# Optimization experiments

Measured on AMD Instinct MI355X. Metric: run time of the kernel, lower is better.

The kernel has to match this reference:

```python
import jax, jax.numpy as jnp
import numpy as np

B, S, P, E, H, NCTX = 4, 1024, 1024, 1024, 16, 2048
D = E // H


def setup_inputs() -> dict:
    key = jax.random.key(0)
    k0, k1, k2, k3 = jax.random.split(key, 4)
    x = jax.random.normal(k0, (B, S, E), jnp.float32)
    layer_past = jax.random.normal(k1, (2, B, H, P, D), jnp.float32)
    w_attn = jax.random.normal(k2, (E, 3 * E), jnp.float32) * 0.02
    b_attn = jnp.zeros((3 * E,), jnp.float32)
    w_proj = jax.random.normal(k3, (E, E), jnp.float32) * 0.02
    b_proj = jnp.zeros((E,), jnp.float32)
    return {"x": x, "layer_past": layer_past, "w_attn": w_attn,
            "b_attn": b_attn, "w_proj": w_proj, "b_proj": b_proj}


def reference(x, layer_past, w_attn, b_attn, w_proj, b_proj):
    # c_attn: Conv1D == linear with weight [nx, nf]
    qkv = x @ w_attn + b_attn                       # [B,S,3E]
    q, k, v = jnp.split(qkv, 3, axis=-1)

    def heads(t):                                   # [B,S,E] -> [B,H,S,D]
        return t.reshape(B, -1, H, D).transpose(0, 2, 1, 3)

    q, k, v = heads(q), heads(k), heads(v)
    # KV-cache concat: layer_past[0] is [B,H,P,D] (module transposes to
    # [B,H,D,P] then concats on last dim; equivalent to concat on seq dim).
    k = jnp.concatenate([layer_past[0], k], axis=2)  # [B,H,ns,D]
    v = jnp.concatenate([layer_past[1], v], axis=2)  # [B,H,ns,D]
    present = jnp.stack([k, v])                      # [2,B,H,ns,D]

    nd, ns = q.shape[2], k.shape[2]
    w = jnp.einsum('bhqd,bhkd->bhqk', q, k) / jnp.sqrt(jnp.float32(D))
    mask = jnp.tril(jnp.ones((NCTX, NCTX), jnp.float32))[ns - nd:ns, :ns]
    w = w * mask - 10000.0 * (1.0 - mask)
    a = jnp.einsum('bhqk,bhkd->bhqd', jax.nn.softmax(w, axis=-1), v)
    a = a.transpose(0, 2, 1, 3).reshape(B, -1, E)    # merge heads
    out = a @ w_proj + b_proj
    return out, present
```

## Files before the change

kernel.cpp:

```cpp
#include <hip/hip_runtime.h>
#include <hip/hip_bf16.h>

#define BB 4
#define SS 1024
#define PP 1024
#define EE 1024
#define HH 16
#define DD 64
#define NS 2048
#define E3 3072
#define VOFF 8388608
#define VPAST 4194304

typedef __attribute__((ext_vector_type(8))) short short8;
typedef __attribute__((ext_vector_type(4))) float floatx4;
typedef __attribute__((ext_vector_type(16))) float floatx16;
typedef __attribute__((ext_vector_type(4))) unsigned uintx4;

__device__ __forceinline__ short f2bf(float f) {
    return (short)(__bfloat16_as_ushort(__float2bfloat16(f)));
}

__device__ __forceinline__ unsigned cvtpk(float lo, float hi) {
    unsigned r;
    asm("v_cvt_pk_bf16_f32 %0, %1, %2" : "=v"(r) : "v"(lo), "v"(hi));
    return r;
}

__device__ __forceinline__ void plswap(unsigned &a, unsigned &b) {
    asm("v_permlane32_swap_b32 %0, %1" : "+v"(a), "+v"(b));
}

__device__ __forceinline__ void gload16(const void* g, void* l) {
    __builtin_amdgcn_global_load_lds(
        (const __attribute__((address_space(1))) void*)g,
        (__attribute__((address_space(3))) void*)l, 16, 0, 0);
}

__global__ __launch_bounds__(256) void cvt_copy_k(
    const float* __restrict__ x, const float* __restrict__ past,
    short* __restrict__ xb, short* __restrict__ kbp, short* __restrict__ vbp,
    float* __restrict__ present)
{
    size_t e0 = ((size_t)blockIdx.x * 256 + threadIdx.x) * 8;
    if (e0 < 4194304) {
        float4 a0 = *(const float4*)(x + e0);
        float4 a1 = *(const float4*)(x + e0 + 4);
        short8 s;
        s[0] = f2bf(a0.x); s[1] = f2bf(a0.y); s[2] = f2bf(a0.z); s[3] = f2bf(a0.w);
        s[4] = f2bf(a1.x); s[5] = f2bf(a1.y); s[6] = f2bf(a1.z); s[7] = f2bf(a1.w);
        *(short8*)(xb + e0) = s;
    } else {
        size_t r = e0 - 4194304;
        int sec = (r >= 4194304);
        if (sec) r -= 4194304;
        const float* src = past + (sec ? VPAST : 0) + r;
        int row = (int)(r >> 6);
        int bh = row >> 10, t = row & 1023, d = (int)(r & 63);
        size_t off = ((size_t)bh * NS + t) * DD + d;
        float4 a0 = *(const float4*)src;
        float4 a1 = *(const float4*)(src + 4);
        short8 s;
        s[0] = f2bf(a0.x); s[1] = f2bf(a0.y); s[2] = f2bf(a0.z); s[3] = f2bf(a0.w);
        s[4] = f2bf(a1.x); s[5] = f2bf(a1.y); s[6] = f2bf(a1.z); s[7] = f2bf(a1.w);
        *(short8*)((sec ? vbp : kbp) + off) = s;
        float* pd = present + (sec ? VOFF : 0) + off;
        *(float4*)(pd)     = a0;
        *(float4*)(pd + 4) = a1;
    }
}

__global__ __launch_bounds__(256) void wtrans_k(
    const float* __restrict__ wa, const float* __restrict__ wp,
    short* __restrict__ wab, short* __restrict__ wpb)
{
    __shared__ short Ts[64][72];
    int bid = blockIdx.x;
    const float* src; short* dst; int n0, k0, Nsrc;
    if (bid < 768) { k0 = (bid & 15) * 64; n0 = (bid >> 4) * 64; src = wa; dst = wab; Nsrc = E3; }
    else { bid -= 768; k0 = (bid & 15) * 64; n0 = (bid >> 4) * 64; src = wp; dst = wpb; Nsrc = EE; }
    int tid = threadIdx.x;
    int r = tid >> 2, c = (tid & 3) * 16;
    const float* s = src + (size_t)(k0 + r) * Nsrc + n0 + c;
    float4 a0 = *(const float4*)(s);
    float4 a1 = *(const float4*)(s + 4);
    float4 a2 = *(const float4*)(s + 8);
    float4 a3 = *(const float4*)(s + 12);
    Ts[c +  0][r] = f2bf(a0.x); Ts[c +  1][r] = f2bf(a0.y);
    Ts[c +  2][r] = f2bf(a0.z); Ts[c +  3][r] = f2bf(a0.w);
    Ts[c +  4][r] = f2bf(a1.x); Ts[c +  5][r] = f2bf(a1.y);
    Ts[c +  6][r] = f2bf(a1.z); Ts[c +  7][r] = f2bf(a1.w);
    Ts[c +  8][r] = f2bf(a2.x); Ts[c +  9][r] = f2bf(a2.y);
    Ts[c + 10][r] = f2bf(a2.z); Ts[c + 11][r] = f2bf(a2.w);
    Ts[c + 12][r] = f2bf(a3.x); Ts[c + 13][r] = f2bf(a3.y);
    Ts[c + 14][r] = f2bf(a3.z); Ts[c + 15][r] = f2bf(a3.w);
    __syncthreads();
    int n = tid >> 2, kc = (tid & 3) * 16;
    short8 v0 = *(const short8*)&Ts[n][kc];
    short8 v1 = *(const short8*)&Ts[n][kc + 8];
    short* d = dst + (size_t)(n0 + n) * EE + k0 + kc;
    *(short8*)d = v0;
    *(short8*)(d + 8) = v1;
}

template<int MODE, int NT>
__global__ __launch_bounds__(256) void gemm_bt_k(
    const short* __restrict__ A,
    const short* __restrict__ Bt,
    const float* __restrict__ bias,
    float* __restrict__ outf,
    short* __restrict__ qb, short* __restrict__ kbp, short* __restrict__ vbp,
    float* __restrict__ present,
    int N)
{
    constexpr int MR = (NT == 128) ? 4 : 2;
    __shared__ __align__(16) short As[128 * 32];
    __shared__ __align__(16) short Bs[NT * 32];
    int tid = threadIdx.x;
    int wave = tid >> 6, lane = tid & 63;
    int fr = lane & 15, quad = lane >> 4;
    int wm = (NT == 128) ? (wave >> 1) : wave;
    int wn = (NT == 128) ? (wave & 1) : 0;
    int hw = blockIdx.y * gridDim.x + blockIdx.x;
    int nwg = gridDim.x * gridDim.y;
    int work = (hw & 7) * (nwg >> 3) + (hw >> 3);
    int bx = work / gridDim.y, by = work - bx * gridDim.y;
    int m0 = bx * 128, n0 = by * NT;

    floatx4 acc[MR][4];
#pragma unroll
    for (int m = 0; m < MR; ++m)
#pragma unroll
        for (int n = 0; n < 4; ++n) acc[m][n] = (floatx4){0.f, 0.f, 0.f, 0.f};

    for (int k0 = 0; k0 < 1024; k0 += 32) {
        __syncthreads();
#pragma unroll
        for (int p = 0; p < 2; ++p) {
            int idx = p * 256 + tid;
            int row = idx >> 2, ch = idx & 3;
            gload16(A + (size_t)(m0 + row) * 1024 + k0 + ch * 8,
                    As + (p * 256 + wave * 64) * 8);
        }
#pragma unroll
        for (int p = 0; p < NT / 64; ++p) {
            int idx = p * 256 + tid;
            int row = idx >> 2, ch = idx & 3;
            gload16(Bt + (size_t)(n0 + row) * 1024 + k0 + ch * 8,
                    Bs + (p * 256 + wave * 64) * 8);
        }
        __syncthreads();
        short8 af[MR], bf[4];
#pragma unroll
        for (int m = 0; m < MR; ++m)
            af[m] = *(const short8*)(As + (wm * (MR * 16) + m * 16 + fr) * 32 + quad * 8);
#pragma unroll
        for (int n = 0; n < 4; ++n)
            bf[n] = *(const short8*)(Bs + (wn * 64 + n * 16 + fr) * 32 + quad * 8);
#pragma unroll
        for (int m = 0; m < MR; ++m)
#pragma unroll
            for (int n = 0; n < 4; ++n)
                acc[m][n] = __builtin_amdgcn_mfma_f32_16x16x32_bf16(af[m], bf[n], acc[m][n], 0, 0, 0);
    }
#pragma unroll
    for (int n = 0; n < 4; ++n) {
        int gc = n0 + wn * 64 + n * 16 + fr;
        float bv = bias[gc];
#pragma unroll
        for (int m = 0; m < MR; ++m) {
#pragma unroll
            for (int r = 0; r < 4; ++r) {
                int gr = m0 + wm * (MR * 16) + m * 16 + quad * 4 + r;
                float val = acc[m][n][r] + bv;
                if (MODE == 1) {
                    outf[(size_t)gr * N + gc] = val;
                } else {
                    int sec = gc >> 10, h = (gc >> 6) & 15, d = gc & 63;
                    int b = gr >> 10, sq = gr & 1023;
                    size_t bh = (size_t)(b * HH + h);
                    if (sec == 0) {
                        qb[(bh * SS + sq) * DD + d] = f2bf(val * 0.18033688f);
                    } else {
                        size_t off = (bh * NS + PP + sq) * DD + d;
                        if (sec == 1) { present[off] = val;        kbp[off] = f2bf(val); }
                        else          { present[VOFF + off] = val; vbp[off] = f2bf(val); }
                    }
                }
            }
        }
    }
}

__global__ __launch_bounds__(256) void flash_attn_k(
    const short* __restrict__ qb, const short* __restrict__ kbp,
    const short* __restrict__ vbp, short* __restrict__ ab)
{
    __shared__ __align__(16) short smem[16384];
    short* Ks = smem;
    short* Vs = smem + 8192;

    int tid = threadIdx.x;
    int wave = tid >> 6, lane = tid & 63;
    int qcol = lane & 31, hi = lane >> 5;

    int bid = blockIdx.x;
    int work = (bid & 7) * 64 + (bid >> 3);
    int bh = work >> 3;
    int q0 = (work & 7) * 128;

    const short* qrow = qb + ((size_t)bh * SS + q0 + wave * 32 + qcol) * DD + hi * 8;
    short8 qf[4];
#pragma unroll
    for (int i = 0; i < 4; ++i) qf[i] = *(const short8*)(qrow + i * 16);

    const short* kbase = kbp + (size_t)bh * NS * DD;
    const short* vbase = vbp + (size_t)bh * NS * DD;

    float m_r = -1e30f, l_r = 0.f;
    floatx16 Oa[2];
#pragma unroll
    for (int dt = 0; dt < 2; ++dt)
#pragma unroll
        for (int r = 0; r < 16; ++r) Oa[dt][r] = 0.f;

    int vkey = lane, vd0 = (tid >> 6) * 16;
    int qminw = PP + q0 + wave * 32;
    int qmaxw = qminw + 31;

    int nchunks = 18 + (q0 >> 6);
    short8 vs0, vs1;

    auto KISSUE = [&](int cc, int bufi) {
        const short* kc = kbase + (size_t)cc * 64 * DD;
        short* Kd = Ks + bufi * 4096;
#pragma unroll
        for (int p = 0; p < 2; ++p) {
            int idx = p * 256 + tid;
            int row = idx >> 3, ch = idx & 7;
            gload16(kc + row * 64 + ((ch ^ (row & 7)) * 8), Kd + (p * 256 + wave * 64) * 8);
        }
    };
    auto VLOAD = [&](int cc) {
        const short* src = vbase + ((size_t)cc * 64 + vkey) * DD + vd0;
        vs0 = *(const short8*)src;
        vs1 = *(const short8*)(src + 8);
    };
    auto VWRITE = [&](int bufi) {
        short* Vd = Vs + bufi * 4096;
#pragma unroll
        for (int i = 0; i < 8; ++i) {
            int d0i = vd0 + i, d1i = vd0 + 8 + i;
            Vd[d0i * 64 + (((vkey >> 3) ^ (d0i & 7)) << 3) + (vkey & 7)] = vs0[i];
            Vd[d1i * 64 + (((vkey >> 3) ^ (d1i & 7)) << 3) + (vkey & 7)] = vs1[i];
        }
    };

    KISSUE(0, 0); VLOAD(0); VWRITE(0);
    __syncthreads();

    for (int c = 0; c < nchunks; ++c) {
        int t0 = c * 64;
        int cur = c & 1;
        KISSUE(c + 1, cur ^ 1);
        VLOAD(c + 1);
        if (t0 <= qmaxw) {
            const short* Kc = Ks + cur * 4096;
            const short* Vc = Vs + cur * 4096;
            floatx16 Sa[2];
#pragma unroll
            for (int ct = 0; ct < 2; ++ct)
#pragma unroll
                for (int r = 0; r < 16; ++r) Sa[ct][r] = 0.f;
#pragma unroll
            for (int ct = 0; ct < 2; ++ct) {
                int key = ct * 32 + qcol;
                int rbase = key * 64, rx = key & 7;
#pragma unroll
                for (int d0 = 0; d0 < 4; ++d0) {
                    short8 kf = *(const short8*)(Kc + rbase + (((d0 * 2 + hi) ^ rx) * 8));
                    Sa[ct] = __builtin_amdgcn_mfma_f32_32x32x16_bf16(kf, qf[d0], Sa[ct], 0, 0, 0);
                }
            }
            if (t0 + 63 > qminw) {
                int qa = qminw + qcol;
#pragma unroll
                for (int ct = 0; ct < 2; ++ct)
#pragma unroll
                    for (int r = 0; r < 16; ++r) {
                        int ka = t0 + ct * 32 + (r & 3) + 8 * (r >> 2) + 4 * hi;
                        if (ka > qa) Sa[ct][r] = -1e30f;
                    }
            }
            float mx0 = Sa[0][0], mx1 = Sa[0][1], mx2 = Sa[0][2], mx3 = Sa[0][3];
#pragma unroll
            for (int ct = 0; ct < 2; ++ct)
#pragma unroll
                for (int r = (ct ? 0 : 4); r < 16; r += 4) {
                    mx0 = fmaxf(mx0, Sa[ct][r]);
                    mx1 = fmaxf(mx1, Sa[ct][r + 1]);
                    mx2 = fmaxf(mx2, Sa[ct][r + 2]);
                    mx3 = fmaxf(mx3, Sa[ct][r + 3]);
                }
            float mx = fmaxf(fmaxf(mx0, mx1), fmaxf(mx2, mx3));
            mx = fmaxf(mx, __shfl_xor(mx, 32, 64));
            if (!__all(mx <= m_r + 11.5416f)) {
                float mnew = fmaxf(m_r, mx);
                float al = exp2f(m_r - mnew);
                l_r *= al;
#pragma unroll
                for (int dt = 0; dt < 2; ++dt)
#pragma unroll
                    for (int r = 0; r < 16; ++r) Oa[dt][r] *= al;
                m_r = mnew;
            }
            float s0 = 0.f, s1 = 0.f, s2 = 0.f, s3 = 0.f;
#pragma unroll
            for (int ct = 0; ct < 2; ++ct)
#pragma unroll
                for (int r = 0; r < 16; r += 4) {
                    float p0 = exp2f(Sa[ct][r]     - m_r);
                    float p1 = exp2f(Sa[ct][r + 1] - m_r);
                    float p2 = exp2f(Sa[ct][r + 2] - m_r);
                    float p3 = exp2f(Sa[ct][r + 3] - m_r);
                    Sa[ct][r] = p0; Sa[ct][r + 1] = p1; Sa[ct][r + 2] = p2; Sa[ct][r + 3] = p3;
                    s0 += p0; s1 += p1; s2 += p2; s3 += p3;
                }
            float sum = (s0 + s1) + (s2 + s3);
            sum += __shfl_xor(sum, 32, 64);
            l_r += sum;
            short8 pfr[2][2];
#pragma unroll
            for (int ct = 0; ct < 2; ++ct) {
                unsigned w0 = cvtpk(Sa[ct][0],  Sa[ct][1]);
                unsigned w2 = cvtpk(Sa[ct][4],  Sa[ct][5]);
                unsigned w1 = cvtpk(Sa[ct][2],  Sa[ct][3]);
                unsigned w3 = cvtpk(Sa[ct][6],  Sa[ct][7]);
                plswap(w0, w2);
                plswap(w1, w3);
                union { uintx4 u; short8 s; } cv0;
                cv0.u = (uintx4){w0, w1, w2, w3};
                pfr[ct][0] = cv0.s;
                unsigned x0 = cvtpk(Sa[ct][8],  Sa[ct][9]);
                unsigned x2 = cvtpk(Sa[ct][12], Sa[ct][13]);
                unsigned x1 = cvtpk(Sa[ct][10], Sa[ct][11]);
                unsigned x3 = cvtpk(Sa[ct][14], Sa[ct][15]);
                plswap(x0, x2);
                plswap(x1, x3);
                union { uintx4 u; short8 s; } cv1;
                cv1.u = (uintx4){x0, x1, x2, x3};
                pfr[ct][1] = cv1.s;
            }
#pragma unroll
            for (int ct = 0; ct < 2; ++ct)
#pragma unroll
                for (int ks = 0; ks < 2; ++ks) {
                    int chunkb = ct * 4 + ks * 2 + hi;
#pragma unroll
                    for (int dt = 0; dt < 2; ++dt) {
                        int row = dt * 32 + qcol;
                        short8 vf = *(const short8*)(Vc + row * 64 + ((chunkb ^ (row & 7)) << 3));
                        Oa[dt] = __builtin_amdgcn_mfma_f32_32x32x16_bf16(vf, pfr[ct][ks], Oa[dt], 0, 0, 0);
                    }
                }
        }
        VWRITE(cur ^ 1);
        __syncthreads();
    }
    short* Ow = smem + wave * 2304;
    float inv = 1.f / l_r;
#pragma unroll
    for (int dt = 0; dt < 2; ++dt)
#pragma unroll
        for (int r = 0; r < 16; ++r) {
            int d = dt * 32 + (r & 3) + 8 * (r >> 2) + 4 * hi;
            Ow[qcol * 72 + d] = f2bf(Oa[dt][r] * inv);
        }
    int b = bh >> 4, h = bh & 15;
    int row = lane >> 1, doff = (lane & 1) * 32;
    int qa = q0 + wave * 32 + row;
    short* dst = ab + ((size_t)(b * SS + qa)) * EE + h * DD + doff;
    const short* srcr = Ow + row * 72 + doff;
    *(short8*)(dst)      = *(const short8*)(srcr);
    *(short8*)(dst + 8)  = *(const short8*)(srcr + 8);
    *(short8*)(dst + 16) = *(const short8*)(srcr + 16);
    *(short8*)(dst + 24) = *(const short8*)(srcr + 24);
}

extern "C" void kernel_launch(void* const* d_in, const int* in_sizes, int n_in,
                              void* d_out, int out_size, void* d_ws, size_t ws_size,
                              hipStream_t stream) {
    const float* x      = (const float*)d_in[0];
    const float* past   = (const float*)d_in[1];
    const float* w_attn = (const float*)d_in[2];
    const float* b_attn = (const float*)d_in[3];
    const float* w_proj = (const float*)d_in[4];
    const float* b_proj = (const float*)d_in[5];
    float* out = (float*)d_out;
    float* present = out + (size_t)BB * SS * EE;

    short* ws  = (short*)d_ws;
    short* xb  = ws;
    short* wab = xb  + 4194304;
    short* wpb = wab + 3145728;
    short* qb  = wpb + 1048576;
    short* kbp = qb  + 4194304;
    short* vbp = kbp + 8388608;
    short* ab  = vbp + 8388608;

    cvt_copy_k<<<6144, 256, 0, stream>>>(x, past, xb, kbp, vbp, present);
    wtrans_k<<<1024, 256, 0, stream>>>(w_attn, w_proj, wab, wpb);
    gemm_bt_k<0, 128><<<dim3(32, 24), 256, 0, stream>>>(xb, wab, b_attn, nullptr,
                                                        qb, kbp, vbp, present, E3);
    flash_attn_k<<<512, 256, 0, stream>>>(qb, kbp, vbp, ab);
    gemm_bt_k<1, 64><<<dim3(32, 16), 256, 0, stream>>>(ab, wpb, b_proj, out,
                                                       nullptr, nullptr, nullptr, nullptr, EE);
}
```

Baseline: 302.4 us.

## Split attention keys across wave pairs and double-buffer GEMM LDS tiles

The flash attention block grows to 512 threads. Each pair of waves shares one 32-query group and splits every 64-key chunk into two 32-key halves. Afterward the two partial softmax states (max, sum, output) are merged through shared memory. This doubles the waves per block to raise occupancy and latency hiding, at the cost of an extra reduction epilogue with several barriers. The GEMM kernels now double-buffer their A/B LDS tiles, loading the next k-slice while computing the current one and using one barrier per iteration instead of two, which doubles LDS use.

Result: no change. 297.5 us (-1.6%).

```diff
diff --git a/kernel.cpp b/kernel.cpp
--- a/kernel.cpp
+++ b/kernel.cpp
@@ -114,8 +114,8 @@
     int N)
 {
     constexpr int MR = (NT == 128) ? 4 : 2;
-    __shared__ __align__(16) short As[128 * 32];
-    __shared__ __align__(16) short Bs[NT * 32];
+    __shared__ __align__(16) short As[2][128 * 32];
+    __shared__ __align__(16) short Bs[2][NT * 32];
     int tid = threadIdx.x;
     int wave = tid >> 6, lane = tid & 63;
     int fr = lane & 15, quad = lane >> 4;
@@ -133,35 +133,41 @@
 #pragma unroll
         for (int n = 0; n < 4; ++n) acc[m][n] = (floatx4){0.f, 0.f, 0.f, 0.f};
 
-    for (int k0 = 0; k0 < 1024; k0 += 32) {
-        __syncthreads();
+    auto STAGE = [&](int k0, int buf) {
 #pragma unroll
         for (int p = 0; p < 2; ++p) {
             int idx = p * 256 + tid;
             int row = idx >> 2, ch = idx & 3;
             gload16(A + (size_t)(m0 + row) * 1024 + k0 + ch * 8,
-                    As + (p * 256 + wave * 64) * 8);
+                    &As[buf][(p * 256 + wave * 64) * 8]);
         }
 #pragma unroll
         for (int p = 0; p < NT / 64; ++p) {
             int idx = p * 256 + tid;
             int row = idx >> 2, ch = idx & 3;
             gload16(Bt + (size_t)(n0 + row) * 1024 + k0 + ch * 8,
-                    Bs + (p * 256 + wave * 64) * 8);
+                    &Bs[buf][(p * 256 + wave * 64) * 8]);
         }
-        __syncthreads();
+    };
+
+    STAGE(0, 0);
+    __syncthreads();
+    for (int k0 = 0; k0 < 1024; k0 += 32) {
+        int cur = (k0 >> 5) & 1;
+        if (k0 + 32 < 1024) STAGE(k0 + 32, cur ^ 1);
         short8 af[MR], bf[4];
 #pragma unroll
         for (int m = 0; m < MR; ++m)
-            af[m] = *(const short8*)(As + (wm * (MR * 16) + m * 16 + fr) * 32 + quad * 8);
+            af[m] = *(const short8*)(&As[cur][(wm * (MR * 16) + m * 16 + fr) * 32 + quad * 8]);
 #pragma unroll
         for (int n = 0; n < 4; ++n)
-            bf[n] = *(const short8*)(Bs + (wn * 64 + n * 16 + fr) * 32 + quad * 8);
+            bf[n] = *(const short8*)(&Bs[cur][(wn * 64 + n * 16 + fr) * 32 + quad * 8]);
 #pragma unroll
         for (int m = 0; m < MR; ++m)
 #pragma unroll
             for (int n = 0; n < 4; ++n)
                 acc[m][n] = __builtin_amdgcn_mfma_f32_16x16x32_bf16(af[m], bf[n], acc[m][n], 0, 0, 0);
+        __syncthreads();
     }
 #pragma unroll
     for (int n = 0; n < 4; ++n) {
@@ -192,7 +198,7 @@
     }
 }
 
-__global__ __launch_bounds__(256) void flash_attn_k(
+__global__ __launch_bounds__(512) void flash_attn_k(
     const short* __restrict__ qb, const short* __restrict__ kbp,
     const short* __restrict__ vbp, short* __restrict__ ab)
 {
@@ -203,13 +209,14 @@
     int tid = threadIdx.x;
     int wave = tid >> 6, lane = tid & 63;
     int qcol = lane & 31, hi = lane >> 5;
+    int qg = wave >> 1, kh = wave & 1;
 
     int bid = blockIdx.x;
     int work = (bid & 7) * 64 + (bid >> 3);
     int bh = work >> 3;
     int q0 = (work & 7) * 128;
 
-    const short* qrow = qb + ((size_t)bh * SS + q0 + wave * 32 + qcol) * DD + hi * 8;
+    const short* qrow = qb + ((size_t)bh * SS + q0 + qg * 32 + qcol) * DD + hi * 8;
     short8 qf[4];
 #pragma unroll
     for (int i = 0; i < 4; ++i) qf[i] = *(const short8*)(qrow + i * 16);
@@ -224,84 +231,64 @@
 #pragma unroll
         for (int r = 0; r < 16; ++r) Oa[dt][r] = 0.f;
 
-    int vkey = lane, vd0 = (tid >> 6) * 16;
-    int qminw = PP + q0 + wave * 32;
+    int vkey = tid & 63, vd0 = (tid >> 6) * 8;
+    int qminw = PP + q0 + qg * 32;
     int qmaxw = qminw + 31;
 
-    int nchunks = 18 + (q0 >> 6);
-    short8 vs0, vs1;
-
+    short8 vs0;
     auto KISSUE = [&](int cc, int bufi) {
         const short* kc = kbase + (size_t)cc * 64 * DD;
-        short* Kd = Ks + bufi * 4096;
-#pragma unroll
-        for (int p = 0; p < 2; ++p) {
-            int idx = p * 256 + tid;
-            int row = idx >> 3, ch = idx & 7;
-            gload16(kc + row * 64 + ((ch ^ (row & 7)) * 8), Kd + (p * 256 + wave * 64) * 8);
-        }
+        int row = tid >> 3, ch = tid & 7;
+        gload16(kc + row * 64 + ((ch ^ (row & 7)) * 8),
+                Ks + bufi * 4096 + wave * 512);
     };
     auto VLOAD = [&](int cc) {
-        const short* src = vbase + ((size_t)cc * 64 + vkey) * DD + vd0;
-        vs0 = *(const short8*)src;
-        vs1 = *(const short8*)(src + 8);
+        vs0 = *(const short8*)(vbase + ((size_t)cc * 64 + vkey) * DD + vd0);
     };
     auto VWRITE = [&](int bufi) {
         short* Vd = Vs + bufi * 4096;
 #pragma unroll
         for (int i = 0; i < 8; ++i) {
-            int d0i = vd0 + i, d1i = vd0 + 8 + i;
-            Vd[d0i * 64 + (((vkey >> 3) ^ (d0i & 7)) << 3) + (vkey & 7)] = vs0[i];
-            Vd[d1i * 64 + (((vkey >> 3) ^ (d1i & 7)) << 3) + (vkey & 7)] = vs1[i];
+            int di = vd0 + i;
+            Vd[di * 64 + (((vkey >> 3) ^ (di & 7)) << 3) + (vkey & 7)] = vs0[i];
         }
     };
 
+    int nchunks = 18 + (q0 >> 6);
     KISSUE(0, 0); VLOAD(0); VWRITE(0);
     __syncthreads();
 
     for (int c = 0; c < nchunks; ++c) {
         int t0 = c * 64;
         int cur = c & 1;
-        KISSUE(c + 1, cur ^ 1);
-        VLOAD(c + 1);
+        if (c + 1 < nchunks) { KISSUE(c + 1, cur ^ 1); VLOAD(c + 1); }
         if (t0 <= qmaxw) {
             const short* Kc = Ks + cur * 4096;
             const short* Vc = Vs + cur * 4096;
-            floatx16 Sa[2];
-#pragma unroll
-            for (int ct = 0; ct < 2; ++ct)
-#pragma unroll
-                for (int r = 0; r < 16; ++r) Sa[ct][r] = 0.f;
-#pragma unroll
-            for (int ct = 0; ct < 2; ++ct) {
-                int key = ct * 32 + qcol;
-                int rbase = key * 64, rx = key & 7;
-#pragma unroll
-                for (int d0 = 0; d0 < 4; ++d0) {
-                    short8 kf = *(const short8*)(Kc + rbase + (((d0 * 2 + hi) ^ rx) * 8));
-                    Sa[ct] = __builtin_amdgcn_mfma_f32_32x32x16_bf16(kf, qf[d0], Sa[ct], 0, 0, 0);
-                }
+            floatx16 Sa;
+#pragma unroll
+            for (int r = 0; r < 16; ++r) Sa[r] = 0.f;
+            int key = kh * 32 + qcol;
+            int rbase = key * 64, rx = key & 7;
+#pragma unroll
+            for (int d0 = 0; d0 < 4; ++d0) {
+                short8 kf = *(const short8*)(Kc + rbase + (((d0 * 2 + hi) ^ rx) * 8));
+                Sa = __builtin_amdgcn_mfma_f32_32x32x16_bf16(kf, qf[d0], Sa, 0, 0, 0);
             }
             if (t0 + 63 > qminw) {
                 int qa = qminw + qcol;
 #pragma unroll
-                for (int ct = 0; ct < 2; ++ct)
-#pragma unroll
-                    for (int r = 0; r < 16; ++r) {
-                        int ka = t0 + ct * 32 + (r & 3) + 8 * (r >> 2) + 4 * hi;
-                        if (ka > qa) Sa[ct][r] = -1e30f;
-                    }
-            }
-            float mx0 = Sa[0][0], mx1 = Sa[0][1], mx2 = Sa[0][2], mx3 = Sa[0][3];
-#pragma unroll
-            for (int ct = 0; ct < 2; ++ct)
-#pragma unroll
-                for (int r = (ct ? 0 : 4); r < 16; r += 4) {
-                    mx0 = fmaxf(mx0, Sa[ct][r]);
-                    mx1 = fmaxf(mx1, Sa[ct][r + 1]);
-                    mx2 = fmaxf(mx2, Sa[ct][r + 2]);
-                    mx3 = fmaxf(mx3, Sa[ct][r + 3]);
+                for (int r = 0; r < 16; ++r) {
+                    int ka = t0 + kh * 32 + (r & 3) + 8 * (r >> 2) + 4 * hi;
+                    if (ka > qa) Sa[r] = -1e30f;
                 }
+            }
+            float mx0 = fmaxf(Sa[0], Sa[1]),  mx1 = fmaxf(Sa[2], Sa[3]);
+            float mx2 = fmaxf(Sa[4], Sa[5]),  mx3 = fmaxf(Sa[6], Sa[7]);
+            mx0 = fmaxf(mx0, fmaxf(Sa[8], Sa[9]));
+            mx1 = fmaxf(mx1, fmaxf(Sa[10], Sa[11]));
+            mx2 = fmaxf(mx2, fmaxf(Sa[12], Sa[13]));
+            mx3 = fmaxf(mx3, fmaxf(Sa[14], Sa[15]));
             float mx = fmaxf(fmaxf(mx0, mx1), fmaxf(mx2, mx3));
             mx = fmaxf(mx, __shfl_xor(mx, 32, 64));
             if (!__all(mx <= m_r + 11.5416f)) {
@@ -316,75 +303,106 @@
             }
             float s0 = 0.f, s1 = 0.f, s2 = 0.f, s3 = 0.f;
 #pragma unroll
-            for (int ct = 0; ct < 2; ++ct)
-#pragma unroll
-                for (int r = 0; r < 16; r += 4) {
-                    float p0 = exp2f(Sa[ct][r]     - m_r);
-                    float p1 = exp2f(Sa[ct][r + 1] - m_r);
-                    float p2 = exp2f(Sa[ct][r + 2] - m_r);
-                    float p3 = exp2f(Sa[ct][r + 3] - m_r);
-                    Sa[ct][r] = p0; Sa[ct][r + 1] = p1; Sa[ct][r + 2] = p2; Sa[ct][r + 3] = p3;
-                    s0 += p0; s1 += p1; s2 += p2; s3 += p3;
-                }
+            for (int r = 0; r < 16; r += 4) {
+                float p0 = exp2f(Sa[r]     - m_r);
+                float p1 = exp2f(Sa[r + 1] - m_r);
+                float p2 = exp2f(Sa[r + 2] - m_r);
+                float p3 = exp2f(Sa[r + 3] - m_r);
+                Sa[r] = p0; Sa[r + 1] = p1; Sa[r + 2] = p2; Sa[r + 3] = p3;
+                s0 += p0; s1 += p1; s2 += p2; s3 += p3;
+            }
             float sum = (s0 + s1) + (s2 + s3);
             sum += __shfl_xor(sum, 32, 64);
             l_r += sum;
-            short8 pfr[2][2];
-#pragma unroll
-            for (int ct = 0; ct < 2; ++ct) {
-                unsigned w0 = cvtpk(Sa[ct][0],  Sa[ct][1]);
-                unsigned w2 = cvtpk(Sa[ct][4],  Sa[ct][5]);
-                unsigned w1 = cvtpk(Sa[ct][2],  Sa[ct][3]);
-                unsigned w3 = cvtpk(Sa[ct][6],  Sa[ct][7]);
+            short8 pfr[2];
+            {
+                unsigned w0 = cvtpk(Sa[0],  Sa[1]);
+                unsigned w2 = cvtpk(Sa[4],  Sa[5]);
+                unsigned w1 = cvtpk(Sa[2],  Sa[3]);
+                unsigned w3 = cvtpk(Sa[6],  Sa[7]);
                 plswap(w0, w2);
                 plswap(w1, w3);
                 union { uintx4 u; short8 s; } cv0;
                 cv0.u = (uintx4){w0, w1, w2, w3};
-                pfr[ct][0] = cv0.s;
-                unsigned x0 = cvtpk(Sa[ct][8],  Sa[ct][9]);
-                unsigned x2 = cvtpk(Sa[ct][12], Sa[ct][13]);
-                unsigned x1 = cvtpk(Sa[ct][10], Sa[ct][11]);
-                unsigned x3 = cvtpk(Sa[ct][14], Sa[ct][15]);
+                pfr[0] = cv0.s;
+                unsigned x0 = cvtpk(Sa[8],  Sa[9]);
+                unsigned x2 = cvtpk(Sa[12], Sa[13]);
+                unsigned x1 = cvtpk(Sa[10], Sa[11]);
+                unsigned x3 = cvtpk(Sa[14], Sa[15]);
                 plswap(x0, x2);
                 plswap(x1, x3);
                 union { uintx4 u; short8 s; } cv1;
                 cv1.u = (uintx4){x0, x1, x2, x3};
-                pfr[ct][1] = cv1.s;
-            }
-#pragma unroll
-            for (int ct = 0; ct < 2; ++ct)
-#pragma unroll
-                for (int ks = 0; ks < 2; ++ks) {
-                    int chunkb = ct * 4 + ks * 2 + hi;
-#pragma unroll
-                    for (int dt = 0; dt < 2; ++dt) {
-                        int row = dt * 32 + qcol;
-                        short8 vf = *(const short8*)(Vc + row * 64 + ((chunkb ^ (row & 7)) << 3));
-                        Oa[dt] = __builtin_amdgcn_mfma_f32_32x32x16_bf16(vf, pfr[ct][ks], Oa[dt], 0, 0, 0);
-                    }
+                pfr[1] = cv1.s;
+            }
+#pragma unroll
+            for (int ks = 0; ks < 2; ++ks) {
+                int chunkb = kh * 4 + ks * 2 + hi;
+#pragma unroll
+                for (int dt = 0; dt < 2; ++dt) {
+                    int row = dt * 32 + qcol;
+                    short8 vf = *(const short8*)(Vc + row * 64 + ((chunkb ^ (row & 7)) << 3));
+                    Oa[dt] = __builtin_amdgcn_mfma_f32_32x32x16_bf16(vf, pfr[ks], Oa[dt], 0, 0, 0);
                 }
+            }
         }
-        VWRITE(cur ^ 1);
+        if (c + 1 < nchunks) VWRITE(cur ^ 1);
         __syncthreads();
     }
-    short* Ow = smem + wave * 2304;
-    float inv = 1.f / l_r;
-#pragma unroll
-    for (int dt = 0; dt < 2; ++dt)
-#pragma unroll
-        for (int r = 0; r < 16; ++r) {
-            int d = dt * 32 + (r & 3) + 8 * (r >> 2) + 4 * hi;
-            Ow[qcol * 72 + d] = f2bf(Oa[dt][r] * inv);
-        }
+
+    float* mlf = (float*)smem;
+    if (hi == 0) {
+        mlf[(wave * 32 + qcol) * 2]     = m_r;
+        mlf[(wave * 32 + qcol) * 2 + 1] = l_r;
+    }
+    __syncthreads();
+    float m_o = mlf[((wave ^ 1) * 32 + qcol) * 2];
+    float l_o = mlf[((wave ^ 1) * 32 + qcol) * 2 + 1];
+    __syncthreads();
+    float M = fmaxf(m_r, m_o);
+    float sc = exp2f(m_r - M);
+    float l_tot = l_r * sc + l_o * exp2f(m_o - M);
+    float* Of = (float*)smem;
+    if (kh == 0) {
+#pragma unroll
+        for (int dt = 0; dt < 2; ++dt)
+#pragma unroll
+            for (int r = 0; r < 16; ++r) {
+                int d = dt * 32 + (r & 3) + 8 * (r >> 2) + 4 * hi;
+                Of[(qg * 64 + d) * 32 + qcol] = Oa[dt][r] * sc;
+            }
+    }
+    __syncthreads();
+    if (kh == 1) {
+        float inv = 1.f / l_tot;
+#pragma unroll
+        for (int dt = 0; dt < 2; ++dt)
+#pragma unroll
+            for (int r = 0; r < 16; ++r) {
+                int d = dt * 32 + (r & 3) + 8 * (r >> 2) + 4 * hi;
+                Oa[dt][r] = (Of[(qg * 64 + d) * 32 + qcol] + Oa[dt][r] * sc) * inv;
+            }
+    }
+    __syncthreads();
+    short* Ot = smem;
+    if (kh == 1) {
+#pragma unroll
+        for (int dt = 0; dt < 2; ++dt)
+#pragma unroll
+            for (int r = 0; r < 16; ++r) {
+                int d = dt * 32 + (r & 3) + 8 * (r >> 2) + 4 * hi;
+                Ot[(qg * 32 + qcol) * 72 + d] = f2bf(Oa[dt][r]);
+            }
+    }
+    __syncthreads();
+    int r2 = tid >> 2;
+    int qgi = r2 >> 5, qi = r2 & 31, doff = (tid & 3) * 16;
     int b = bh >> 4, h = bh & 15;
-    int row = lane >> 1, doff = (lane & 1) * 32;
-    int qa = q0 + wave * 32 + row;
+    int qa = q0 + qgi * 32 + qi;
     short* dst = ab + ((size_t)(b * SS + qa)) * EE + h * DD + doff;
-    const short* srcr = Ow + row * 72 + doff;
-    *(short8*)(dst)      = *(const short8*)(srcr);
-    *(short8*)(dst + 8)  = *(const short8*)(srcr + 8);
-    *(short8*)(dst + 16) = *(const short8*)(srcr + 16);
-    *(short8*)(dst + 24) = *(const short8*)(srcr + 24);
+    const short* srcr = Ot + (qgi * 32 + qi) * 72 + doff;
+    *(short8*)(dst)     = *(const short8*)(srcr);
+    *(short8*)(dst + 8) = *(const short8*)(srcr + 8);
 }
 
 extern "C" void kernel_launch(void* const* d_in, const int* in_sizes, int n_in,
@@ -412,7 +430,7 @@
     wtrans_k<<<1024, 256, 0, stream>>>(w_attn, w_proj, wab, wpb);
     gemm_bt_k<0, 128><<<dim3(32, 24), 256, 0, stream>>>(xb, wab, b_attn, nullptr,
                                                         qb, kbp, vbp, present, E3);
-    flash_attn_k<<<512, 256, 0, stream>>>(qb, kbp, vbp, ab);
+    flash_attn_k<<<512, 512, 0, stream>>>(qb, kbp, vbp, ab);
     gemm_bt_k<1, 64><<<dim3(32, 16), 256, 0, stream>>>(ab, wpb, b_proj, out,
                                                        nullptr, nullptr, nullptr, nullptr, EE);
 }
```

## Triple-buffer GEMM loads and split flash attention keys across wave pairs

Applied to the files above, without the earlier changes.

The GEMM now keeps three LDS stages and prefetches two k-tiles ahead, waiting on vmcnt instead of a full barrier pair per step, so global loads overlap the MFMA work. Flash attention now uses 64-query blocks (1024 workgroups, longest causal rows scheduled first). Each pair of waves splits the key chunks by parity and merges its partial softmax state through LDS at the end. This aims to raise occupancy and balance causal work, at the cost of a longer epilogue with extra syncs and more LDS use in the GEMM.

Measured after the change: 311.1 us. 1.03x slower.

```diff
diff --git a/kernel.cpp b/kernel.cpp
--- a/kernel.cpp
+++ b/kernel.cpp
@@ -114,8 +114,8 @@
     int N)
 {
     constexpr int MR = (NT == 128) ? 4 : 2;
-    __shared__ __align__(16) short As[128 * 32];
-    __shared__ __align__(16) short Bs[NT * 32];
+    __shared__ __align__(16) short As[3][128 * 32];
+    __shared__ __align__(16) short Bs[3][NT * 32];
     int tid = threadIdx.x;
     int wave = tid >> 6, lane = tid & 63;
     int fr = lane & 15, quad = lane >> 4;
@@ -133,30 +133,46 @@
 #pragma unroll
         for (int n = 0; n < 4; ++n) acc[m][n] = (floatx4){0.f, 0.f, 0.f, 0.f};
 
-    for (int k0 = 0; k0 < 1024; k0 += 32) {
-        __syncthreads();
+    auto STAGE = [&](int k0, int buf) {
 #pragma unroll
         for (int p = 0; p < 2; ++p) {
             int idx = p * 256 + tid;
             int row = idx >> 2, ch = idx & 3;
             gload16(A + (size_t)(m0 + row) * 1024 + k0 + ch * 8,
-                    As + (p * 256 + wave * 64) * 8);
+                    &As[buf][(p * 256 + wave * 64) * 8]);
         }
 #pragma unroll
         for (int p = 0; p < NT / 64; ++p) {
             int idx = p * 256 + tid;
             int row = idx >> 2, ch = idx & 3;
             gload16(Bt + (size_t)(n0 + row) * 1024 + k0 + ch * 8,
-                    Bs + (p * 256 + wave * 64) * 8);
-        }
-        __syncthreads();
+                    &Bs[buf][(p * 256 + wave * 64) * 8]);
+        }
+    };
+
+    STAGE(0, 0);
+    STAGE(32, 1);
+    for (int t = 0; t < 32; ++t) {
+        if (t < 31) {
+            if (NT == 128) asm volatile("s_waitcnt vmcnt(4)" ::: "memory");
+            else           asm volatile("s_waitcnt vmcnt(3)" ::: "memory");
+        } else {
+            asm volatile("s_waitcnt vmcnt(0)" ::: "memory");
+        }
+        __builtin_amdgcn_s_barrier();
+        asm volatile("" ::: "memory");
+        int cb = t - (t / 3) * 3;
         short8 af[MR], bf[4];
 #pragma unroll
         for (int m = 0; m < MR; ++m)
-            af[m] = *(const short8*)(As + (wm * (MR * 16) + m * 16 + fr) * 32 + quad * 8);
+            af[m] = *(const short8*)(&As[cb][(wm * (MR * 16) + m * 16 + fr) * 32 + quad * 8]);
 #pragma unroll
         for (int n = 0; n < 4; ++n)
-            bf[n] = *(const short8*)(Bs + (wn * 64 + n * 16 + fr) * 32 + quad * 8);
+            bf[n] = *(const short8*)(&Bs[cb][(wn * 64 + n * 16 + fr) * 32 + quad * 8]);
+        if (t + 2 < 32) {
+            int nb = (t + 2) - ((t + 2) / 3) * 3;
+            STAGE((t + 2) * 32, nb);
+        }
 #pragma unroll
         for (int m = 0; m < MR; ++m)
 #pragma unroll
@@ -203,13 +219,16 @@
     int tid = threadIdx.x;
     int wave = tid >> 6, lane = tid & 63;
     int qcol = lane & 31, hi = lane >> 5;
+    int qt = wave >> 1, sp = wave & 1;
 
     int bid = blockIdx.x;
-    int work = (bid & 7) * 64 + (bid >> 3);
-    int bh = work >> 3;
-    int q0 = (work & 7) * 128;
-
-    const short* qrow = qb + ((size_t)bh * SS + q0 + wave * 32 + qcol) * DD + hi * 8;
+    int xcd = bid & 7, s = bid >> 3;
+    int j = 15 - (s >> 3);
+    int bh = xcd * 8 + (s & 7);
+    int q0 = j * 64;
+    int q32 = q0 + qt * 32;
+
+    const short* qrow = qb + ((size_t)bh * SS + q32 + qcol) * DD + hi * 8;
     short8 qf[4];
 #pragma unroll
     for (int i = 0; i < 4; ++i) qf[i] = *(const short8*)(qrow + i * 16);
@@ -224,13 +243,12 @@
 #pragma unroll
         for (int r = 0; r < 16; ++r) Oa[dt][r] = 0.f;
 
-    int vkey = lane, vd0 = (tid >> 6) * 16;
-    int qminw = PP + q0 + wave * 32;
+    int vkey = tid & 63, vd0 = (tid >> 6) * 16;
+    int qminw = PP + q32;
     int qmaxw = qminw + 31;
-
-    int nchunks = 18 + (q0 >> 6);
+    int nchunks = 17 + j;
+
     short8 vs0, vs1;
-
     auto KISSUE = [&](int cc, int bufi) {
         const short* kc = kbase + (size_t)cc * 64 * DD;
         short* Kd = Ks + bufi * 4096;
@@ -256,15 +274,14 @@
         }
     };
 
-    KISSUE(0, 0); VLOAD(0); VWRITE(0);
+    VLOAD(0); KISSUE(0, 0); VWRITE(0);
     __syncthreads();
 
     for (int c = 0; c < nchunks; ++c) {
         int t0 = c * 64;
         int cur = c & 1;
-        KISSUE(c + 1, cur ^ 1);
-        VLOAD(c + 1);
-        if (t0 <= qmaxw) {
+        if (c + 1 < nchunks) { VLOAD(c + 1); KISSUE(c + 1, cur ^ 1); }
+        if (((c ^ sp) & 1) == 0 && t0 <= qmaxw) {
             const short* Kc = Ks + cur * 4096;
             const short* Vc = Vs + cur * 4096;
             floatx16 Sa[2];
@@ -364,27 +381,63 @@
                     }
                 }
         }
-        VWRITE(cur ^ 1);
+        if (c + 1 < nchunks) VWRITE(cur ^ 1);
         __syncthreads();
     }
-    short* Ow = smem + wave * 2304;
-    float inv = 1.f / l_r;
-#pragma unroll
-    for (int dt = 0; dt < 2; ++dt)
-#pragma unroll
-        for (int r = 0; r < 16; ++r) {
-            int d = dt * 32 + (r & 3) + 8 * (r >> 2) + 4 * hi;
-            Ow[qcol * 72 + d] = f2bf(Oa[dt][r] * inv);
-        }
+
+    float* mlf = (float*)smem;
+    if (hi == 0) {
+        mlf[(wave * 32 + qcol) * 2]     = m_r;
+        mlf[(wave * 32 + qcol) * 2 + 1] = l_r;
+    }
+    __syncthreads();
+    float m_o = mlf[((wave ^ 1) * 32 + qcol) * 2];
+    float l_o = mlf[((wave ^ 1) * 32 + qcol) * 2 + 1];
+    __syncthreads();
+    float M = fmaxf(m_r, m_o);
+    float sc = exp2f(m_r - M);
+    float l_tot = l_r * sc + l_o * exp2f(m_o - M);
+    float* Of = (float*)smem;
+    if (sp == 0) {
+#pragma unroll
+        for (int dt = 0; dt < 2; ++dt)
+#pragma unroll
+            for (int r = 0; r < 16; ++r) {
+                int d = dt * 32 + (r & 3) + 8 * (r >> 2) + 4 * hi;
+                Of[(qt * 64 + d) * 32 + qcol] = Oa[dt][r] * sc;
+            }
+    }
+    __syncthreads();
+    if (sp == 1) {
+        float inv = 1.f / l_tot;
+#pragma unroll
+        for (int dt = 0; dt < 2; ++dt)
+#pragma unroll
+            for (int r = 0; r < 16; ++r) {
+                int d = dt * 32 + (r & 3) + 8 * (r >> 2) + 4 * hi;
+                Oa[dt][r] = (Of[(qt * 64 + d) * 32 + qcol] + Oa[dt][r] * sc) * inv;
+            }
+    }
+    __syncthreads();
+    short* Ot = smem;
+    if (sp == 1) {
+#pragma unroll
+        for (int dt = 0; dt < 2; ++dt)
+#pragma unroll
+            for (int r = 0; r < 16; ++r) {
+                int d = dt * 32 + (r & 3) + 8 * (r >> 2) + 4 * hi;
+                Ot[(qt * 32 + qcol) * 72 + d] = f2bf(Oa[dt][r]);
+            }
+    }
+    __syncthreads();
+    int r2 = tid >> 2;
+    int qgi = r2 >> 5, qi = r2 & 31, doff = (tid & 3) * 16;
     int b = bh >> 4, h = bh & 15;
-    int row = lane >> 1, doff = (lane & 1) * 32;
-    int qa = q0 + wave * 32 + row;
+    int qa = q0 + qgi * 32 + qi;
     short* dst = ab + ((size_t)(b * SS + qa)) * EE + h * DD + doff;
-    const short* srcr = Ow + row * 72 + doff;
-    *(short8*)(dst)      = *(const short8*)(srcr);
-    *(short8*)(dst + 8)  = *(const short8*)(srcr + 8);
-    *(short8*)(dst + 16) = *(const short8*)(srcr + 16);
-    *(short8*)(dst + 24) = *(const short8*)(srcr + 24);
+    const short* srcr = Ot + (qgi * 32 + qi) * 72 + doff;
+    *(short8*)(dst)     = *(const short8*)(srcr);
+    *(short8*)(dst + 8) = *(const short8*)(srcr + 8);
 }
 
 extern "C" void kernel_launch(void* const* d_in, const int* in_sizes, int n_in,
@@ -412,7 +465,7 @@
     wtrans_k<<<1024, 256, 0, stream>>>(w_attn, w_proj, wab, wpb);
     gemm_bt_k<0, 128><<<dim3(32, 24), 256, 0, stream>>>(xb, wab, b_attn, nullptr,
                                                         qb, kbp, vbp, present, E3);
-    flash_attn_k<<<512, 256, 0, stream>>>(qb, kbp, vbp, ab);
+    flash_attn_k<<<1024, 256, 0, stream>>>(qb, kbp, vbp, ab);
     gemm_bt_k<1, 64><<<dim3(32, 16), 256, 0, stream>>>(ab, wpb, b_proj, out,
                                                        nullptr, nullptr, nullptr, nullptr, EE);
 }
```
